# Kernel optimization log

Measured on AMD Instinct MI355X. Metric: run time of the kernel, lower is better.

Reference implementation:

```python
import jax, jax.numpy as jnp
import numpy as np

NUM_CODES = 4096
EMBED_DIM = 64
BETA = 0.25


def setup_inputs() -> dict:
    key = jax.random.key(0)
    k1, k2 = jax.random.split(key)
    z = jax.random.normal(k1, (8, EMBED_DIM, 64, 64), dtype=jnp.float32)
    weight = jax.random.normal(k2, (NUM_CODES, EMBED_DIM), dtype=jnp.float32)
    return {"z": z, "weight": weight}


def reference(z, weight):
    # z: [B, C, H, W] -> [B, H, W, C]
    z_bhwc = jnp.moveaxis(z, 1, -1)
    z_flat = z_bhwc.reshape(-1, EMBED_DIM)  # [N, d]

    # squared-euclidean distances: ||z||^2 + ||w||^2 - 2 z.w  -> [N, num_codes]
    distance = (
        jnp.sum(z_flat ** 2, axis=1, keepdims=True)
        + jnp.sum(weight ** 2, axis=1)
        - 2.0 * jnp.einsum('bd,nd->bn', z_flat, weight)
    )
    encoding_indices = jnp.argmin(distance, axis=1)  # [N]

    # codebook lookup (gather)
    z_q = weight[encoding_indices].reshape(z_bhwc.shape)  # [B, H, W, C]

    encodings = jax.nn.one_hot(encoding_indices, NUM_CODES, dtype=z.dtype)  # [N, num_codes]
    avg_probs = jnp.mean(encodings, axis=0)
    tiny = 1e-10  # max(1e-10, finfo(fp32).tiny)
    perplexity = jnp.exp(-jnp.sum(avg_probs * jnp.log(avg_probs + tiny)))

    # commitment loss (z_q detached) — eval path, no EMA state update
    loss = BETA * jnp.mean((jax.lax.stop_gradient(z_q) - z_bhwc) ** 2)

    # straight-through estimator
    z_q = z_bhwc + jax.lax.stop_gradient(z_q - z_bhwc)
    z_q = jnp.moveaxis(z_q, -1, 1)  # back to [B, C, H, W]

    return z_q, loss, perplexity, encodings, encoding_indices
```

## Files before the change

### kernel.cpp

```cpp
#include <hip/hip_runtime.h>
#include <math.h>
#include <float.h>

#define ZQ_OFF   0
#define LOSS_OFF 2097152
#define PERP_OFF 2097153
#define ENC_OFF  2097154
#define IDX_OFF  136314882ULL
#define BETA     0.25f


typedef __attribute__((ext_vector_type(8))) short short8;
typedef __attribute__((ext_vector_type(4))) float f32x4;
typedef __attribute__((ext_vector_type(2))) float f32x2;

#define MFMA16(a, b, c) __builtin_amdgcn_mfma_f32_16x16x32_bf16(a, b, c, 0, 0, 0)

__device__ __forceinline__ float bf16_rn(float v, unsigned short* h) {
    unsigned u = __float_as_uint(v);
    unsigned r = (u + 0x7fffu + ((u >> 16) & 1u)) & 0xffff0000u;
    *h = (unsigned short)(r >> 16);
    return __uint_as_float(r);
}
__device__ __forceinline__ void split3(float v, unsigned short* h, unsigned short* m, unsigned short* l) {
    float hf = bf16_rn(v, h);
    float r1 = v - hf;
    float mf = bf16_rn(r1, m);
    float r2 = r1 - mf;
    bf16_rn(r2, l);
}

__global__ void vq_wnorm(const float* __restrict__ w, float* __restrict__ wnorm) {
    int c = blockIdx.x * 256 + threadIdx.x;
    const float4* w4 = (const float4*)(w + ((size_t)c << 6));
    float s = 0.f;
    #pragma unroll
    for (int k = 0; k < 16; ++k) { float4 v = w4[k]; s += v.x*v.x + v.y*v.y + v.z*v.z + v.w*v.w; }
    wnorm[c] = s;
}

__global__ void vq_prep(const float* __restrict__ w, unsigned short* __restrict__ w3) {
    int u = blockIdx.x * 256 + threadIdx.x;
    int c = u >> 5, slot = u & 31;
    if (slot >= 24) return;
    int p = slot >> 3, g = slot & 7;
    float4 v0 = *(const float4*)(w + ((size_t)c << 6) + g * 8);
    float4 v1 = *(const float4*)(w + ((size_t)c << 6) + g * 8 + 4);
    float vv[8] = {v0.x, v0.y, v0.z, v0.w, v1.x, v1.y, v1.z, v1.w};
    short8 o;
    #pragma unroll
    for (int e = 0; e < 8; ++e) {
        unsigned short h, m, l;
        split3(vv[e], &h, &m, &l);
        o[e] = (short)((p == 0) ? h : (p == 1) ? m : l);
    }
    size_t db = (size_t)((((c >> 4) * 3 + p) * 2 + (g >> 2)) * 4 + (g & 3)) * 256
              + (size_t)(c & 15) * 16;
    *(short8*)((char*)w3 + db) = o;
}

__global__ __launch_bounds__(256, 3) void vq_main(
    const float* __restrict__ z, const float* __restrict__ w,
    const float* __restrict__ wnorm, const unsigned short* __restrict__ w3,
    float* __restrict__ out,
    float* __restrict__ loss_ws, int* __restrict__ ticket, int* __restrict__ hist)
{
    __shared__ __align__(16) char wl[2 * 12288];
    __shared__ float snorm[4096];
    __shared__ int s_widx[64];
    __shared__ int s_flag;

    const int tx    = threadIdx.x;
    const int lane  = tx & 63;
    const int wv    = tx >> 6;
    const int rh    = wv & 1;
    const int chalf = wv >> 1;
    const int lcol  = lane & 15;
    const int lkq   = lane >> 4;
    const int base  = blockIdx.x * 64;
    const int bb    = base >> 12;
    const int hh    = (base & 4095) >> 6;

    const char* w3b = (const char*)w3;

    float (*zS)[64] = (float (*)[64])wl;
    #pragma unroll
    for (int j = 0; j < 4; ++j) {
        int f4 = j * 256 + tx;
        int d  = f4 >> 4, w4i = f4 & 15;
        float4 v = *(const float4*)(z + (((size_t)bb * 64 + d) * 64 + hh) * 64 + w4i * 4);
        *(float4*)&zS[d][w4i * 4] = v;
    }
    #pragma unroll
    for (int j = 0; j < 4; ++j) {
        int c4 = (j * 256 + tx) * 4;
        *(float4*)&snorm[c4] = *(const float4*)(wnorm + c4);
    }
    __syncthreads();

    short8 aH[2][2], aM[2][2], aL[2][2];
    #pragma unroll
    for (int u = 0; u < 2; ++u)
        #pragma unroll
        for (int s = 0; s < 2; ++s)
            #pragma unroll
            for (int j = 0; j < 8; ++j) {
                float v = zS[s * 32 + lkq * 8 + j][rh * 32 + u * 16 + lcol];
                unsigned short h, m, l;
                split3(v, &h, &m, &l);
                aH[u][s][j] = (short)h; aM[u][s][j] = (short)m; aL[u][s][j] = (short)l;
            }
    __builtin_amdgcn_sched_barrier(0);
    __builtin_amdgcn_s_barrier();
    __builtin_amdgcn_sched_barrier(0);

    {
        const char* s0 = w3b + wv * 3072 + (size_t)lane * 16;
        char* d0 = wl + wv * 3072;
        #pragma unroll
        for (int i = 0; i < 3; ++i)
            __builtin_amdgcn_global_load_lds(
                (const __attribute__((address_space(1))) void*)(s0 + i * 1024),
                (__attribute__((address_space(3))) void*)(d0 + i * 1024), 16, 0, 0);
    }
    __builtin_amdgcn_sched_barrier(0);
    asm volatile("s_waitcnt vmcnt(0)" ::: "memory");
    __builtin_amdgcn_s_barrier();
    __builtin_amdgcn_sched_barrier(0);

    float best[2][4]; int bidx[2][4];
    #pragma unroll
    for (int u = 0; u < 2; ++u)
        #pragma unroll
        for (int r = 0; r < 4; ++r) { best[u][r] = FLT_MAX; bidx[u][r] = 0; }

    float* enc = out + ENC_OFF;
    const f32x2 zero2 = {0.f, 0.f};

    #pragma unroll 1
    for (int ch = 0; ch < 128; ++ch) {
        char* nxt = wl + (~ch & 1) * 12288;

        {
            const char* s0 = w3b + (size_t)((ch + 1) & 127) * 12288 + wv * 3072
                           + (size_t)lane * 16;
            char* d0 = nxt + wv * 3072;
            #pragma unroll
            for (int i = 0; i < 3; ++i)
                __builtin_amdgcn_global_load_lds(
                    (const __attribute__((address_space(1))) void*)(s0 + i * 1024),
                    (__attribute__((address_space(3))) void*)(d0 + i * 1024), 16, 0, 0);
        }
        __builtin_amdgcn_sched_barrier(0);
        {
            f32x2* rowp = (f32x2*)(enc + ((size_t)(base + (ch >> 1)) << 12));
            #pragma unroll
            for (int j = 0; j < 4; ++j) {
                int slot = (ch & 1) * 1024 + ((j * 256 + tx + 7) & 1023);
                __builtin_nontemporal_store(zero2, rowp + slot);
            }
        }
        __builtin_amdgcn_sched_barrier(0);
        asm volatile("s_waitcnt vmcnt(11)" ::: "memory");
        __builtin_amdgcn_s_barrier();
        __builtin_amdgcn_sched_barrier(0);

        {
            const int code0 = ch * 32 + chalf * 16;
            const char* bufc = wl + (ch & 1) * 12288 + chalf * 6144 + (size_t)lane * 16;
            short8 bH0 = *(const short8*)(bufc);
            short8 bH1 = *(const short8*)(bufc + 1024);
            short8 bM0 = *(const short8*)(bufc + 2048);
            short8 bM1 = *(const short8*)(bufc + 3072);
            short8 bL0 = *(const short8*)(bufc + 4096);
            short8 bL1 = *(const short8*)(bufc + 5120);
            const float wnv = snorm[code0 + lcol];
            #pragma unroll
            for (int u = 0; u < 2; ++u) {
                f32x4 c0 = {0.f,0.f,0.f,0.f}, c1 = {0.f,0.f,0.f,0.f}, c2 = {0.f,0.f,0.f,0.f};
                c0 = MFMA16(aH[u][0], bH0, c0); c0 = MFMA16(aH[u][1], bH1, c0);
                c1 = MFMA16(aH[u][0], bM0, c1); c1 = MFMA16(aH[u][1], bM1, c1);
                c1 = MFMA16(aM[u][0], bH0, c1); c1 = MFMA16(aM[u][1], bH1, c1);
                c2 = MFMA16(aM[u][0], bM0, c2); c2 = MFMA16(aM[u][1], bM1, c2);
                c2 = MFMA16(aH[u][0], bL0, c2); c2 = MFMA16(aH[u][1], bL1, c2);
                c2 = MFMA16(aL[u][0], bH0, c2); c2 = MFMA16(aL[u][1], bH1, c2);
                #pragma unroll
                for (int r = 0; r < 4; ++r) {
                    float sdot = (c0[r] + c1[r]) + c2[r];
                    float dd = fmaf(-2.f, sdot, wnv);
                    if (dd < best[u][r]) { best[u][r] = dd; bidx[u][r] = code0 + lcol; }
                }
            }
        }
        __builtin_amdgcn_sched_barrier(0);
        __builtin_amdgcn_s_barrier();
    }

    __syncthreads();

    #pragma unroll
    for (int u = 0; u < 2; ++u)
        #pragma unroll
        for (int mm = 1; mm < 16; mm <<= 1)
            #pragma unroll
            for (int r = 0; r < 4; ++r) {
                float ob = __shfl_xor(best[u][r], mm, 64);
                int   oi = __shfl_xor(bidx[u][r], mm, 64);
                if (ob < best[u][r] || (ob == best[u][r] && oi < bidx[u][r])) {
                    best[u][r] = ob; bidx[u][r] = oi;
                }
            }

    float2* s_red = (float2*)snorm;
    if (lcol == 0) {
        #pragma unroll
        for (int u = 0; u < 2; ++u)
            #pragma unroll
            for (int r = 0; r < 4; ++r) {
                int row = rh * 32 + u * 16 + lkq * 4 + r;
                s_red[row * 2 + chalf] = make_float2(best[u][r], __int_as_float(bidx[u][r]));
            }
    }
    __syncthreads();

    if (tx < 64) {
        float2 a = s_red[tx * 2], b2 = s_red[tx * 2 + 1];
        int ai = __float_as_int(a.y), bi2 = __float_as_int(b2.y);
        int bi;
        if (a.x < b2.x || (a.x == b2.x && ai < bi2)) bi = ai; else bi = bi2;
        s_widx[tx] = bi;
        __builtin_nontemporal_store((float)bi, out + IDX_OFF + (size_t)(base + tx));
        atomicAdd(&hist[bi], 1);
        enc[((size_t)(base + tx) << 12) + bi] = 1.0f;
    }
    __syncthreads();

    {
        const int row = tx & 63;
        const int dg  = tx >> 6;
        const int wi  = s_widx[row];
        const float* qrow = w + ((size_t)wi << 6);
        float lsum = 0.f;
        #pragma unroll
        for (int dd = 0; dd < 16; ++dd) {
            int d = dg * 16 + dd;
            float qv = qrow[d];
            float zv = z[(((size_t)bb * 64 + d) * 64 + hh) * 64 + row];
            float diff = qv - zv;
            lsum += diff * diff;
            __builtin_nontemporal_store(zv + (qv - zv),
                out + ZQ_OFF + (((size_t)bb * 64 + d) * 64 + hh) * 64 + row);
        }
        #pragma unroll
        for (int off = 32; off > 0; off >>= 1) lsum += __shfl_down(lsum, off, 64);
        if ((tx & 63) == 0) atomicAdd(loss_ws, lsum);
    }

    __syncthreads();
    if (tx == 0) {
        __threadfence();
        int old = atomicAdd(ticket, 1);
        s_flag = (old == 511) ? 1 : 0;
    }
    __syncthreads();
    if (s_flag) {
        __threadfence();
        float s = 0.f;
        #pragma unroll
        for (int j = 0; j < 16; ++j) {
            int c = tx + j * 256;
            int cnt = atomicAdd(&hist[c], 0);
            float p = (float)cnt * (1.f / 32768.f);
            s += p * logf(p + 1e-10f);
        }
        float* fr = snorm;
        fr[tx] = s;
        __syncthreads();
        for (int off = 128; off > 0; off >>= 1) {
            if (tx < off) fr[tx] += fr[tx + off];
            __syncthreads();
        }
        if (tx == 0) {
            out[LOSS_OFF] = BETA * atomicAdd(loss_ws, 0.f) / 2097152.f;
            out[PERP_OFF] = expf(-fr[0]);
        }
    }
}

extern "C" void kernel_launch(void* const* d_in, const int* in_sizes, int n_in,
                              void* d_out, int out_size, void* d_ws, size_t ws_size,
                              hipStream_t stream)
{
    const float* z = (const float*)d_in[0];
    const float* w = (const float*)d_in[1];
    float* out     = (float*)d_out;
    float* loss_ws = (float*)d_ws;
    int*   ticket  = (int*)((char*)d_ws + 4);
    int*   hist    = (int*)((char*)d_ws + 16);
    float* wnorm   = (float*)((char*)d_ws + 16400);
    unsigned short* w3 = (unsigned short*)((char*)d_ws + 32800);
    (void)ws_size; (void)in_sizes; (void)n_in; (void)out_size;

    hipMemsetAsync(d_ws, 0, 16 + 4096 * sizeof(int), stream);
    vq_wnorm<<<16, 256, 0, stream>>>(w, wnorm);
    vq_prep<<<512, 256, 0, stream>>>(w, w3);
    vq_main<<<512, 256, 0, stream>>>(z, w, wnorm, w3, out, loss_ws, ticket, hist);
}
```

Measured before the change: 623.8 us.

## Use per-wave 4-deep LDS ring for codebook prefetch without block barriers

Replaces the block-shared double buffer of codebook bf16 slices with a private 4-slot LDS ring per wave, prefetching three chunks ahead and synchronising only with vmcnt waits. This removes the two s_barriers per iteration and deepens latency hiding. It also keeps z in a dedicated LDS tile so the epilogue reads z from LDS instead of global memory. The cost is a much larger LDS footprint (about 96KB ring), so launch bounds drop to one block per SIMD-set occupancy, and each wave now loads its own copy of the codebook slices, doubling global-to-LDS traffic.

```diff
diff --git a/kernel.cpp b/kernel.cpp
--- a/kernel.cpp
+++ b/kernel.cpp
@@ -59,13 +59,14 @@
     *(short8*)((char*)w3 + db) = o;
 }
 
-__global__ __launch_bounds__(256, 3) void vq_main(
+__global__ __launch_bounds__(256, 1) void vq_main(
     const float* __restrict__ z, const float* __restrict__ w,
     const float* __restrict__ wnorm, const unsigned short* __restrict__ w3,
     float* __restrict__ out,
     float* __restrict__ loss_ws, int* __restrict__ ticket, int* __restrict__ hist)
 {
-    __shared__ __align__(16) char wl[2 * 12288];
+    __shared__ __align__(16) char ring[4 * 4 * 6144];
+    __shared__ float zS[64][64];
     __shared__ float snorm[4096];
     __shared__ int s_widx[64];
     __shared__ int s_flag;
@@ -81,9 +82,20 @@
     const int bb    = base >> 12;
     const int hh    = (base & 4095) >> 6;
 
-    const char* w3b = (const char*)w3;
-
-    float (*zS)[64] = (float (*)[64])wl;
+    const char* wsrc = (const char*)w3 + (size_t)lane * 16;
+    char* ringw = ring + wv * 24576;
+
+    #pragma unroll
+    for (int p = 0; p < 3; ++p) {
+        const char* s0 = wsrc + (size_t)(p * 2 + chalf) * 6144;
+        char* d0 = ringw + p * 6144;
+        #pragma unroll
+        for (int i = 0; i < 6; ++i)
+            __builtin_amdgcn_global_load_lds(
+                (const __attribute__((address_space(1))) void*)(s0 + i * 1024),
+                (__attribute__((address_space(3))) void*)(d0 + i * 1024), 16, 0, 0);
+    }
+
     #pragma unroll
     for (int j = 0; j < 4; ++j) {
         int f4 = j * 256 + tx;
@@ -110,23 +122,6 @@
                 split3(v, &h, &m, &l);
                 aH[u][s][j] = (short)h; aM[u][s][j] = (short)m; aL[u][s][j] = (short)l;
             }
-    __builtin_amdgcn_sched_barrier(0);
-    __builtin_amdgcn_s_barrier();
-    __builtin_amdgcn_sched_barrier(0);
-
-    {
-        const char* s0 = w3b + wv * 3072 + (size_t)lane * 16;
-        char* d0 = wl + wv * 3072;
-        #pragma unroll
-        for (int i = 0; i < 3; ++i)
-            __builtin_amdgcn_global_load_lds(
-                (const __attribute__((address_space(1))) void*)(s0 + i * 1024),
-                (__attribute__((address_space(3))) void*)(d0 + i * 1024), 16, 0, 0);
-    }
-    __builtin_amdgcn_sched_barrier(0);
-    asm volatile("s_waitcnt vmcnt(0)" ::: "memory");
-    __builtin_amdgcn_s_barrier();
-    __builtin_amdgcn_sched_barrier(0);
 
     float best[2][4]; int bidx[2][4];
     #pragma unroll
@@ -138,36 +133,33 @@
     const f32x2 zero2 = {0.f, 0.f};
 
     #pragma unroll 1
-    for (int ch = 0; ch < 128; ++ch) {
-        char* nxt = wl + (~ch & 1) * 12288;
-
+    for (int k = 0; k < 128; ++k) {
+        const int slot = k & 3;
         {
-            const char* s0 = w3b + (size_t)((ch + 1) & 127) * 12288 + wv * 3072
-                           + (size_t)lane * 16;
-            char* d0 = nxt + wv * 3072;
-            #pragma unroll
-            for (int i = 0; i < 3; ++i)
+            const char* s0 = wsrc + (size_t)((((k + 3) & 127) * 2 + chalf)) * 6144;
+            char* d0 = ringw + ((k + 3) & 3) * 6144;
+            #pragma unroll
+            for (int i = 0; i < 6; ++i)
                 __builtin_amdgcn_global_load_lds(
                     (const __attribute__((address_space(1))) void*)(s0 + i * 1024),
                     (__attribute__((address_space(3))) void*)(d0 + i * 1024), 16, 0, 0);
         }
         __builtin_amdgcn_sched_barrier(0);
         {
-            f32x2* rowp = (f32x2*)(enc + ((size_t)(base + (ch >> 1)) << 12));
+            f32x2* rowp = (f32x2*)(enc + ((size_t)(base + (k >> 1)) << 12));
             #pragma unroll
             for (int j = 0; j < 4; ++j) {
-                int slot = (ch & 1) * 1024 + ((j * 256 + tx + 7) & 1023);
-                __builtin_nontemporal_store(zero2, rowp + slot);
+                int slt = (k & 1) * 1024 + ((j * 256 + tx + 7) & 1023);
+                __builtin_nontemporal_store(zero2, rowp + slt);
             }
         }
         __builtin_amdgcn_sched_barrier(0);
-        asm volatile("s_waitcnt vmcnt(11)" ::: "memory");
-        __builtin_amdgcn_s_barrier();
+        asm volatile("s_waitcnt vmcnt(34)" ::: "memory");
         __builtin_amdgcn_sched_barrier(0);
 
         {
-            const int code0 = ch * 32 + chalf * 16;
-            const char* bufc = wl + (ch & 1) * 12288 + chalf * 6144 + (size_t)lane * 16;
+            const int code0 = k * 32 + chalf * 16;
+            const char* bufc = ringw + slot * 6144 + (size_t)lane * 16;
             short8 bH0 = *(const short8*)(bufc);
             short8 bH1 = *(const short8*)(bufc + 1024);
             short8 bM0 = *(const short8*)(bufc + 2048);
@@ -192,8 +184,6 @@
                 }
             }
         }
-        __builtin_amdgcn_sched_barrier(0);
-        __builtin_amdgcn_s_barrier();
     }
 
     __syncthreads();
@@ -245,7 +235,7 @@
         for (int dd = 0; dd < 16; ++dd) {
             int d = dg * 16 + dd;
             float qv = qrow[d];
-            float zv = z[(((size_t)bb * 64 + d) * 64 + hh) * 64 + row];
+            float zv = zS[d][row];
             float diff = qv - zv;
             lsum += diff * diff;
             __builtin_nontemporal_store(zv + (qv - zv),
```

Measured after the change: 672.4 us. +7.8%, slower.
